# Kernel tuning notes

Measured on AMD Instinct MI355X. Metric: run time of the kernel, lower is better.

## Reference

```python
import jax, jax.numpy as jnp
import numpy as np

N_CLASS = 5      # episode way
SHOTS = 5        # support images per class
D = 64           # local descriptor dim (feature_dim)
H = W = 16       # feature map spatial size
N_QUERY = 75     # 15 queries per class


def setup_inputs() -> dict:
    key = jax.random.key(0)
    k1, k2 = jax.random.split(key)
    support = jax.random.normal(k1, (N_CLASS * SHOTS, D, H, W), dtype=jnp.float32)
    query = jax.random.normal(k2, (N_QUERY, D, H, W), dtype=jnp.float32)
    return {"support": support, "query": query, "task_index": 0, "k": 3, "k2": 64}


def reference(support, query, task_index, k, k2):
    C = N_CLASS
    n, d, h, w = support.shape
    hw = h * w
    ns = n // C  # shots per class

    # Per-class support descriptors: [C, ns*h*w, d], L2-normalized along d
    s = support.reshape(C, ns, d, hw)
    s = jnp.transpose(s, (0, 1, 3, 2)).reshape(C, ns * hw, d)
    s = s / jnp.linalg.norm(s, axis=-1, keepdims=True)

    # Query local descriptors: [B, d, Nq], L2-normalized along d
    B = query.shape[0]
    q = query.reshape(B, d, -1)
    q = q / jnp.linalg.norm(q, axis=1, keepdims=True)

    # Cosine similarity per class: [C, B, Nq, M]  (M = ns*h*w support descriptors)
    sim = jnp.einsum('cmd,bdq->cbqm', s, q)

    # torch.topk(sim, k, dim=1): top-k over support descriptors M per query location
    v = jax.lax.top_k(sim, k)[0]          # [C, B, Nq, k]
    v = jnp.swapaxes(v, 2, 3)             # [C, B, k, Nq]
    # torch.topk(., k2, dim=2): top-k2 over query locations
    v = jax.lax.top_k(v, k2)[0]           # [C, B, k, k2]

    # cat over classes, unsqueeze, then view(-1, 1, k, k2)
    return v.reshape(-1, 1, k, k2)        # [C*B, 1, k, k2]
```

## Files before the change

### kernel.cpp

```cpp
#include <hip/hip_runtime.h>
#include <stdint.h>


#define C_CLS 5
#define SHOTS 5
#define DIM 64
#define HW 256
#define NQ 75
#define K1 3
#define K2 64
#define M_TOT 1280
#define MPARTS 2
#define MPART 640
#define NIT 5
#define QBLK 128
#define NTILES 150

using bf16x8 = __attribute__((ext_vector_type(8))) short;
using f32x4  = __attribute__((ext_vector_type(4))) float;

typedef __attribute__((address_space(1))) const unsigned int GU32;
typedef __attribute__((address_space(3))) unsigned int LU32;

__device__ __forceinline__ void gload16(const void* g, void* l) {
    __builtin_amdgcn_global_load_lds((GU32*)g, (LU32*)l, 16, 0, 0);
}

#define SWZ(o) ((o) ^ ((((o) >> 7) & 7) << 4))

__device__ inline unsigned short f2bf(float x) {
    uint32_t u = __float_as_uint(x);
    u += 0x7FFF + ((u >> 16) & 1);
    return (unsigned short)(u >> 16);
}

__device__ __forceinline__ void ins3(float v, float& t0, float& t1, float& t2) {
    t2 = __builtin_amdgcn_fmed3f(v, t1, t2);
    t1 = __builtin_amdgcn_fmed3f(v, t0, t1);
    t0 = fmaxf(t0, v);
}

__global__ __launch_bounds__(256)
void prep(const float* __restrict__ support, const float* __restrict__ query,
          unsigned short* __restrict__ Sn, unsigned short* __restrict__ Qn) {
    const int tid  = threadIdx.x;
    const int wv   = tid >> 6, lane = tid & 63;
    const int dg   = lane >> 4, dl = lane & 15;
    const int bid  = blockIdx.x;
    const float* src;
    unsigned short* dst;
    if (bid < NQ * 4) {
        const int b    = bid >> 2;
        const int desc = (bid & 3) * 64 + wv * 16 + dl;
        src = query + (size_t)b * DIM * HW + desc;
        dst = Qn + ((size_t)b * HW + desc) * DIM + dg * 16;
    } else {
        const int sb   = bid - NQ * 4;
        const int cs   = sb >> 2;
        const int desc = (sb & 3) * 64 + wv * 16 + dl;
        const int c = cs / SHOTS, s = cs % SHOTS;
        src = support + (size_t)cs * DIM * HW + desc;
        dst = Sn + ((size_t)c * M_TOT + s * HW + desc) * DIM + dg * 16;
    }
    float v[16];
    float nrm = 0.f;
#pragma unroll
    for (int i = 0; i < 16; ++i) {
        const float x = src[(dg * 16 + i) * HW];
        v[i] = x; nrm = fmaf(x, x, nrm);
    }
    nrm += __shfl_xor(nrm, 16, 64);
    nrm += __shfl_xor(nrm, 32, 64);
    const float inv = rsqrtf(nrm);
    uint32_t p[8];
#pragma unroll
    for (int j = 0; j < 8; ++j)
        p[j] = (uint32_t)f2bf(v[2 * j] * inv) | ((uint32_t)f2bf(v[2 * j + 1] * inv) << 16);
    const uint4 w0 = {p[0], p[1], p[2], p[3]}, w1 = {p[4], p[5], p[6], p[7]};
    ((uint4*)dst)[0] = w0;
    ((uint4*)dst)[1] = w1;
}

__global__ __launch_bounds__(256, 6)
void dn4_mfma(const unsigned short* __restrict__ Sn,
              const unsigned short* __restrict__ Qn,
              unsigned short* __restrict__ partial) {
    __shared__ unsigned short sB[128 * DIM];

    const int tid  = threadIdx.x;
    const int lane = tid & 63, w = tid >> 6;
    const int c15  = lane & 15, kg = lane >> 4;
    const int bid  = blockIdx.x;
    const int c    = bid / 300;
    const int rem  = bid % 300;
    const int part = rem / NTILES;
    const int nt   = rem % NTILES;

    const int q0 = nt * QBLK + w * 32;
    bf16x8 aq[2][2];
#pragma unroll
    for (int g = 0; g < 2; ++g) {
        const unsigned short* qp = Qn + (size_t)(q0 + g * 16 + c15) * DIM + kg * 8;
        aq[g][0] = *(const bf16x8*)qp;
        aq[g][1] = *(const bf16x8*)(qp + 32);
    }

    float t0[2][4], t1[2][4], t2[2][4];
#pragma unroll
    for (int g = 0; g < 2; ++g)
#pragma unroll
        for (int r = 0; r < 4; ++r) { t0[g][r] = -2.f; t1[g][r] = -2.f; t2[g][r] = -2.f; }

    const int sw   = (c15 & 7) << 4;
    const int off0 = (kg * 16) ^ sw;
    const int off1 = (kg * 16 + 64) ^ sw;
    const int rowb = c15 * 128;

    const unsigned short* tb0 =
        Sn + ((size_t)c * M_TOT + part * MPART) * DIM;

    for (int it = 0; it < NIT; ++it) {
        __syncthreads();
        {
            const char* tb = (const char*)(tb0 + (size_t)it * 128 * DIM);
#pragma unroll
            for (int rep = 0; rep < 4; ++rep) {
                const int o = rep * 4096 + w * 1024 + lane * 16;
                gload16(tb + SWZ(o), (char*)sB + rep * 4096 + w * 1024);
            }
        }
        __syncthreads();

#pragma unroll
        for (int ns = 0; ns < 8; ++ns) {
            const char* rp = (const char*)sB + rowb + ns * 2048;
            const bf16x8 b0 = *(const bf16x8*)(rp + off0);
            const bf16x8 b1 = *(const bf16x8*)(rp + off1);
#pragma unroll
            for (int g = 0; g < 2; ++g) {
                f32x4 acc = {0.f, 0.f, 0.f, 0.f};
                acc = __builtin_amdgcn_mfma_f32_16x16x32_bf16(aq[g][0], b0, acc, 0, 0, 0);
                acc = __builtin_amdgcn_mfma_f32_16x16x32_bf16(aq[g][1], b1, acc, 0, 0, 0);
#pragma unroll
                for (int r = 0; r < 4; ++r)
                    ins3(acc[r], t0[g][r], t1[g][r], t2[g][r]);
            }
        }
    }

#pragma unroll
    for (int g = 0; g < 2; ++g)
#pragma unroll
        for (int r = 0; r < 4; ++r)
#pragma unroll
            for (int off = 1; off < 16; off <<= 1) {
                const float o0 = __shfl_xor(t0[g][r], off, 64);
                const float o1 = __shfl_xor(t1[g][r], off, 64);
                const float o2 = __shfl_xor(t2[g][r], off, 64);
                ins3(o0, t0[g][r], t1[g][r], t2[g][r]);
                ins3(o1, t0[g][r], t1[g][r], t2[g][r]);
                ins3(o2, t0[g][r], t1[g][r], t2[g][r]);
            }

    if (c15 == 0) {
        const int b = nt >> 1;
        unsigned short* pbase =
            partial + (((size_t)(c * NQ + b) * MPARTS + part) * K1) * HW;
#pragma unroll
        for (int g = 0; g < 2; ++g)
#pragma unroll
            for (int r = 0; r < 4; ++r) {
                const int qloc = (nt & 1) * QBLK + w * 32 + g * 16 + kg * 4 + r;
                pbase[qloc]          = f2bf(t0[g][r]);
                pbase[HW + qloc]     = f2bf(t1[g][r]);
                pbase[2 * HW + qloc] = f2bf(t2[g][r]);
            }
    }
}

__global__ __launch_bounds__(256)
void dn4_topq(const unsigned short* __restrict__ partial, float* __restrict__ out) {
    __shared__ float sbuf[HW];
    const int tid = threadIdx.x;
    const int bid = blockIdx.x;
    const int ki  = bid % K1;
    const int cb  = bid / K1;

    const unsigned short* p = partial + (size_t)cb * MPARTS * K1 * HW + tid;
    float t0 = -2.f, t1 = -2.f, t2 = -2.f;
#pragma unroll
    for (int h = 0; h < MPARTS; ++h)
#pragma unroll
        for (int r = 0; r < K1; ++r) {
            const float v = __uint_as_float((uint32_t)p[(h * K1 + r) * HW] << 16);
            ins3(v, t0, t1, t2);
        }
    float v = (ki == 0) ? t0 : (ki == 1) ? t1 : t2;

#pragma unroll
    for (int kk = 2; kk <= HW; kk <<= 1) {
#pragma unroll
        for (int j = kk >> 1; j > 0; j >>= 1) {
            const bool keep_max = (((tid & kk) == 0) == ((tid & j) == 0));
            float wv;
            if (j >= 64) {
                sbuf[tid] = v;
                __syncthreads();
                wv = sbuf[tid ^ j];
                __syncthreads();
            } else {
                wv = __shfl_xor(v, j, 64);
            }
            v = keep_max ? fmaxf(v, wv) : fminf(v, wv);
        }
    }
    if (tid < K2) out[(size_t)cb * K1 * K2 + (size_t)ki * K2 + tid] = v;
}

extern "C" void kernel_launch(void* const* d_in, const int* in_sizes, int n_in,
                              void* d_out, int out_size, void* d_ws, size_t ws_size,
                              hipStream_t stream) {
    const float* support = (const float*)d_in[0];
    const float* query   = (const float*)d_in[1];
    float* out = (float*)d_out;

    char* ws = (char*)d_ws;
    unsigned short* Sn      = (unsigned short*)ws;
    unsigned short* Qn      = (unsigned short*)(ws + 819200);
    unsigned short* partial = (unsigned short*)(ws + 819200 + 2457600);

    prep    <<<dim3(400),                      dim3(256), 0, stream>>>(support, query, Sn, Qn);
    dn4_mfma<<<dim3(C_CLS * MPARTS * NTILES),  dim3(256), 0, stream>>>(Sn, Qn, partial);
    dn4_topq<<<dim3(C_CLS * NQ * K1),          dim3(256), 0, stream>>>(partial, out);
}
```

Before: 46.40 us.

## Fuse similarity top-k and query top-k2 into one double-buffered kernel

Merges the MFMA similarity kernel and the query-location top-k2 kernel, so each block handles a full (class, query image) pair over all 1280 support descriptors. This removes the bf16 partial-results buffer, one kernel launch, and the M-split merge step. Support tiles are now double-buffered in LDS so the next tile's load overlaps the current tile's compute. The trade-off is far fewer blocks (375 instead of 1500 plus 1125), more registers per thread with QG=4, and three serial bitonic sorts per block.

```diff
diff --git a/kernel.cpp b/kernel.cpp
--- a/kernel.cpp
+++ b/kernel.cpp
@@ -10,11 +10,8 @@
 #define K1 3
 #define K2 64
 #define M_TOT 1280
-#define MPARTS 2
-#define MPART 640
-#define NIT 5
-#define QBLK 128
-#define NTILES 150
+#define NIT 10
+#define QG 4
 
 using bf16x8 = __attribute__((ext_vector_type(8))) short;
 using f32x4  = __attribute__((ext_vector_type(4))) float;
@@ -81,33 +78,30 @@
     ((uint4*)dst)[1] = w1;
 }
 
-__global__ __launch_bounds__(256, 6)
-void dn4_mfma(const unsigned short* __restrict__ Sn,
-              const unsigned short* __restrict__ Qn,
-              unsigned short* __restrict__ partial) {
-    __shared__ unsigned short sB[128 * DIM];
+__global__ __launch_bounds__(256)
+void dn4_fused(const unsigned short* __restrict__ Sn,
+               const unsigned short* __restrict__ Qn,
+               float* __restrict__ out) {
+    __shared__ unsigned short sB[2][128 * DIM];
 
     const int tid  = threadIdx.x;
     const int lane = tid & 63, w = tid >> 6;
     const int c15  = lane & 15, kg = lane >> 4;
     const int bid  = blockIdx.x;
-    const int c    = bid / 300;
-    const int rem  = bid % 300;
-    const int part = rem / NTILES;
-    const int nt   = rem % NTILES;
-
-    const int q0 = nt * QBLK + w * 32;
-    bf16x8 aq[2][2];
-#pragma unroll
-    for (int g = 0; g < 2; ++g) {
+    const int c    = bid / NQ, b = bid % NQ;
+
+    bf16x8 aq[QG][2];
+    const int q0 = b * HW + w * (QG * 16);
+#pragma unroll
+    for (int g = 0; g < QG; ++g) {
         const unsigned short* qp = Qn + (size_t)(q0 + g * 16 + c15) * DIM + kg * 8;
         aq[g][0] = *(const bf16x8*)qp;
         aq[g][1] = *(const bf16x8*)(qp + 32);
     }
 
-    float t0[2][4], t1[2][4], t2[2][4];
-#pragma unroll
-    for (int g = 0; g < 2; ++g)
+    float t0[QG][4], t1[QG][4], t2[QG][4];
+#pragma unroll
+    for (int g = 0; g < QG; ++g)
 #pragma unroll
         for (int r = 0; r < 4; ++r) { t0[g][r] = -2.f; t1[g][r] = -2.f; t2[g][r] = -2.f; }
 
@@ -116,28 +110,32 @@
     const int off1 = (kg * 16 + 64) ^ sw;
     const int rowb = c15 * 128;
 
-    const unsigned short* tb0 =
-        Sn + ((size_t)c * M_TOT + part * MPART) * DIM;
-
+    const char* tb0 = (const char*)(Sn + (size_t)c * M_TOT * DIM);
+
+#pragma unroll
+    for (int rep = 0; rep < 4; ++rep) {
+        const int o = rep * 4096 + tid * 16;
+        gload16(tb0 + SWZ(o), (char*)sB[0] + rep * 4096 + w * 1024);
+    }
+    __syncthreads();
+
+    int cur = 0;
     for (int it = 0; it < NIT; ++it) {
-        __syncthreads();
-        {
-            const char* tb = (const char*)(tb0 + (size_t)it * 128 * DIM);
+        if (it < NIT - 1) {
+            const char* tb = tb0 + (size_t)(it + 1) * 16384;
 #pragma unroll
             for (int rep = 0; rep < 4; ++rep) {
-                const int o = rep * 4096 + w * 1024 + lane * 16;
-                gload16(tb + SWZ(o), (char*)sB + rep * 4096 + w * 1024);
+                const int o = rep * 4096 + tid * 16;
+                gload16(tb + SWZ(o), (char*)sB[cur ^ 1] + rep * 4096 + w * 1024);
             }
         }
-        __syncthreads();
-
 #pragma unroll
         for (int ns = 0; ns < 8; ++ns) {
-            const char* rp = (const char*)sB + rowb + ns * 2048;
+            const char* rp = (const char*)sB[cur] + rowb + ns * 2048;
             const bf16x8 b0 = *(const bf16x8*)(rp + off0);
             const bf16x8 b1 = *(const bf16x8*)(rp + off1);
 #pragma unroll
-            for (int g = 0; g < 2; ++g) {
+            for (int g = 0; g < QG; ++g) {
                 f32x4 acc = {0.f, 0.f, 0.f, 0.f};
                 acc = __builtin_amdgcn_mfma_f32_16x16x32_bf16(aq[g][0], b0, acc, 0, 0, 0);
                 acc = __builtin_amdgcn_mfma_f32_16x16x32_bf16(aq[g][1], b1, acc, 0, 0, 0);
@@ -146,10 +144,12 @@
                     ins3(acc[r], t0[g][r], t1[g][r], t2[g][r]);
             }
         }
-    }
-
-#pragma unroll
-    for (int g = 0; g < 2; ++g)
+        __syncthreads();
+        cur ^= 1;
+    }
+
+#pragma unroll
+    for (int g = 0; g < QG; ++g)
 #pragma unroll
         for (int r = 0; r < 4; ++r)
 #pragma unroll
@@ -162,59 +162,43 @@
                 ins3(o2, t0[g][r], t1[g][r], t2[g][r]);
             }
 
+    float* sr = (float*)sB;
+    float* xb = sr + K1 * HW;
     if (c15 == 0) {
-        const int b = nt >> 1;
-        unsigned short* pbase =
-            partial + (((size_t)(c * NQ + b) * MPARTS + part) * K1) * HW;
-#pragma unroll
-        for (int g = 0; g < 2; ++g)
+#pragma unroll
+        for (int g = 0; g < QG; ++g)
 #pragma unroll
             for (int r = 0; r < 4; ++r) {
-                const int qloc = (nt & 1) * QBLK + w * 32 + g * 16 + kg * 4 + r;
-                pbase[qloc]          = f2bf(t0[g][r]);
-                pbase[HW + qloc]     = f2bf(t1[g][r]);
-                pbase[2 * HW + qloc] = f2bf(t2[g][r]);
-            }
-    }
-}
-
-__global__ __launch_bounds__(256)
-void dn4_topq(const unsigned short* __restrict__ partial, float* __restrict__ out) {
-    __shared__ float sbuf[HW];
-    const int tid = threadIdx.x;
-    const int bid = blockIdx.x;
-    const int ki  = bid % K1;
-    const int cb  = bid / K1;
-
-    const unsigned short* p = partial + (size_t)cb * MPARTS * K1 * HW + tid;
-    float t0 = -2.f, t1 = -2.f, t2 = -2.f;
-#pragma unroll
-    for (int h = 0; h < MPARTS; ++h)
-#pragma unroll
-        for (int r = 0; r < K1; ++r) {
-            const float v = __uint_as_float((uint32_t)p[(h * K1 + r) * HW] << 16);
-            ins3(v, t0, t1, t2);
+                const int qloc = w * (QG * 16) + g * 16 + kg * 4 + r;
+                sr[0 * HW + qloc] = t0[g][r];
+                sr[1 * HW + qloc] = t1[g][r];
+                sr[2 * HW + qloc] = t2[g][r];
+            }
+    }
+    __syncthreads();
+
+    const size_t obase = (size_t)bid * K1 * K2;
+    for (int rk = 0; rk < K1; ++rk) {
+        float v = sr[rk * HW + tid];
+#pragma unroll
+        for (int kk = 2; kk <= HW; kk <<= 1) {
+#pragma unroll
+            for (int j = kk >> 1; j > 0; j >>= 1) {
+                const bool keep_max = (((tid & kk) == 0) == ((tid & j) == 0));
+                float pw;
+                if (j >= 64) {
+                    xb[tid] = v;
+                    __syncthreads();
+                    pw = xb[tid ^ j];
+                    __syncthreads();
+                } else {
+                    pw = __shfl_xor(v, j, 64);
+                }
+                v = keep_max ? fmaxf(v, pw) : fminf(v, pw);
+            }
         }
-    float v = (ki == 0) ? t0 : (ki == 1) ? t1 : t2;
-
-#pragma unroll
-    for (int kk = 2; kk <= HW; kk <<= 1) {
-#pragma unroll
-        for (int j = kk >> 1; j > 0; j >>= 1) {
-            const bool keep_max = (((tid & kk) == 0) == ((tid & j) == 0));
-            float wv;
-            if (j >= 64) {
-                sbuf[tid] = v;
-                __syncthreads();
-                wv = sbuf[tid ^ j];
-                __syncthreads();
-            } else {
-                wv = __shfl_xor(v, j, 64);
-            }
-            v = keep_max ? fmaxf(v, wv) : fminf(v, wv);
-        }
-    }
-    if (tid < K2) out[(size_t)cb * K1 * K2 + (size_t)ki * K2 + tid] = v;
+        if (tid < K2) out[obase + (size_t)rk * K2 + tid] = v;
+    }
 }
 
 extern "C" void kernel_launch(void* const* d_in, const int* in_sizes, int n_in,
@@ -225,11 +209,9 @@
     float* out = (float*)d_out;
 
     char* ws = (char*)d_ws;
-    unsigned short* Sn      = (unsigned short*)ws;
-    unsigned short* Qn      = (unsigned short*)(ws + 819200);
-    unsigned short* partial = (unsigned short*)(ws + 819200 + 2457600);
-
-    prep    <<<dim3(400),                      dim3(256), 0, stream>>>(support, query, Sn, Qn);
-    dn4_mfma<<<dim3(C_CLS * MPARTS * NTILES),  dim3(256), 0, stream>>>(Sn, Qn, partial);
-    dn4_topq<<<dim3(C_CLS * NQ * K1),          dim3(256), 0, stream>>>(partial, out);
-}
+    unsigned short* Sn = (unsigned short*)ws;
+    unsigned short* Qn = (unsigned short*)(ws + 819200);
+
+    prep     <<<dim3(400),          dim3(256), 0, stream>>>(support, query, Sn, Qn);
+    dn4_fused<<<dim3(C_CLS * NQ),   dim3(256), 0, stream>>>(Sn, Qn, out);
+}
```

Result: slower. 54.15 us (+16.7%).

## Double-buffer support tiles and split support rows four ways with 512-thread blocks

Applied to the files above, without the earlier changes.

The similarity kernel now uses 512-thread blocks that each cover a whole query image (256 locations) against a quarter of a class's support descriptors. It prefetches the next 64-row support tile into a second LDS buffer while the current tile feeds the MFMAs, so each iteration needs one barrier instead of two. The top-k reduction now merges four partial top-3 lists instead of two. This is meant to hide global-to-LDS latency and raise support-tile reuse across more query rows, at the cost of more partial output and a larger merge step.

```diff
diff --git a/kernel.cpp b/kernel.cpp
--- a/kernel.cpp
+++ b/kernel.cpp
@@ -10,11 +10,11 @@
 #define K1 3
 #define K2 64
 #define M_TOT 1280
-#define MPARTS 2
-#define MPART 640
-#define NIT 5
-#define QBLK 128
-#define NTILES 150
+#define MQ 4
+#define MQROWS (M_TOT / MQ)
+#define TROWS 64
+#define NIT (MQROWS / TROWS)
+#define QG 2
 
 using bf16x8 = __attribute__((ext_vector_type(8))) short;
 using f32x4  = __attribute__((ext_vector_type(4))) float;
@@ -81,33 +81,32 @@
     ((uint4*)dst)[1] = w1;
 }
 
-__global__ __launch_bounds__(256, 6)
+__global__ __launch_bounds__(512)
 void dn4_mfma(const unsigned short* __restrict__ Sn,
               const unsigned short* __restrict__ Qn,
               unsigned short* __restrict__ partial) {
-    __shared__ unsigned short sB[128 * DIM];
+    __shared__ unsigned short sB[2][TROWS * DIM];
 
     const int tid  = threadIdx.x;
     const int lane = tid & 63, w = tid >> 6;
     const int c15  = lane & 15, kg = lane >> 4;
     const int bid  = blockIdx.x;
-    const int c    = bid / 300;
-    const int rem  = bid % 300;
-    const int part = rem / NTILES;
-    const int nt   = rem % NTILES;
-
-    const int q0 = nt * QBLK + w * 32;
-    bf16x8 aq[2][2];
-#pragma unroll
-    for (int g = 0; g < 2; ++g) {
+    const int b    = bid % NQ;
+    const int cq   = bid / NQ;
+    const int c    = cq >> 2, qt = cq & 3;
+
+    bf16x8 aq[QG][2];
+    const int q0 = b * HW + w * (QG * 16);
+#pragma unroll
+    for (int g = 0; g < QG; ++g) {
         const unsigned short* qp = Qn + (size_t)(q0 + g * 16 + c15) * DIM + kg * 8;
         aq[g][0] = *(const bf16x8*)qp;
         aq[g][1] = *(const bf16x8*)(qp + 32);
     }
 
-    float t0[2][4], t1[2][4], t2[2][4];
-#pragma unroll
-    for (int g = 0; g < 2; ++g)
+    float t0[QG][4], t1[QG][4], t2[QG][4];
+#pragma unroll
+    for (int g = 0; g < QG; ++g)
 #pragma unroll
         for (int r = 0; r < 4; ++r) { t0[g][r] = -2.f; t1[g][r] = -2.f; t2[g][r] = -2.f; }
 
@@ -116,28 +115,24 @@
     const int off1 = (kg * 16 + 64) ^ sw;
     const int rowb = c15 * 128;
 
-    const unsigned short* tb0 =
-        Sn + ((size_t)c * M_TOT + part * MPART) * DIM;
-
+    const char* tb0 = (const char*)(Sn + ((size_t)c * M_TOT + qt * MQROWS) * DIM);
+
+    gload16(tb0 + SWZ(tid * 16), (char*)sB[0] + w * 1024);
+    __syncthreads();
+
+    int cur = 0;
     for (int it = 0; it < NIT; ++it) {
-        __syncthreads();
-        {
-            const char* tb = (const char*)(tb0 + (size_t)it * 128 * DIM);
-#pragma unroll
-            for (int rep = 0; rep < 4; ++rep) {
-                const int o = rep * 4096 + w * 1024 + lane * 16;
-                gload16(tb + SWZ(o), (char*)sB + rep * 4096 + w * 1024);
-            }
-        }
-        __syncthreads();
-
-#pragma unroll
-        for (int ns = 0; ns < 8; ++ns) {
-            const char* rp = (const char*)sB + rowb + ns * 2048;
+        if (it < NIT - 1) {
+            const char* tb = tb0 + (size_t)(it + 1) * (TROWS * DIM * 2);
+            gload16(tb + SWZ(tid * 16), (char*)sB[cur ^ 1] + w * 1024);
+        }
+#pragma unroll
+        for (int ns = 0; ns < 4; ++ns) {
+            const char* rp = (const char*)sB[cur] + rowb + ns * 2048;
             const bf16x8 b0 = *(const bf16x8*)(rp + off0);
             const bf16x8 b1 = *(const bf16x8*)(rp + off1);
 #pragma unroll
-            for (int g = 0; g < 2; ++g) {
+            for (int g = 0; g < QG; ++g) {
                 f32x4 acc = {0.f, 0.f, 0.f, 0.f};
                 acc = __builtin_amdgcn_mfma_f32_16x16x32_bf16(aq[g][0], b0, acc, 0, 0, 0);
                 acc = __builtin_amdgcn_mfma_f32_16x16x32_bf16(aq[g][1], b1, acc, 0, 0, 0);
@@ -146,10 +141,12 @@
                     ins3(acc[r], t0[g][r], t1[g][r], t2[g][r]);
             }
         }
-    }
-
-#pragma unroll
-    for (int g = 0; g < 2; ++g)
+        __syncthreads();
+        cur ^= 1;
+    }
+
+#pragma unroll
+    for (int g = 0; g < QG; ++g)
 #pragma unroll
         for (int r = 0; r < 4; ++r)
 #pragma unroll
@@ -163,14 +160,13 @@
             }
 
     if (c15 == 0) {
-        const int b = nt >> 1;
         unsigned short* pbase =
-            partial + (((size_t)(c * NQ + b) * MPARTS + part) * K1) * HW;
-#pragma unroll
-        for (int g = 0; g < 2; ++g)
+            partial + (((size_t)(c * NQ + b) * MQ + qt) * K1) * HW;
+#pragma unroll
+        for (int g = 0; g < QG; ++g)
 #pragma unroll
             for (int r = 0; r < 4; ++r) {
-                const int qloc = (nt & 1) * QBLK + w * 32 + g * 16 + kg * 4 + r;
+                const int qloc = w * (QG * 16) + g * 16 + kg * 4 + r;
                 pbase[qloc]          = f2bf(t0[g][r]);
                 pbase[HW + qloc]     = f2bf(t1[g][r]);
                 pbase[2 * HW + qloc] = f2bf(t2[g][r]);
@@ -186,10 +182,10 @@
     const int ki  = bid % K1;
     const int cb  = bid / K1;
 
-    const unsigned short* p = partial + (size_t)cb * MPARTS * K1 * HW + tid;
+    const unsigned short* p = partial + (size_t)cb * MQ * K1 * HW + tid;
     float t0 = -2.f, t1 = -2.f, t2 = -2.f;
 #pragma unroll
-    for (int h = 0; h < MPARTS; ++h)
+    for (int h = 0; h < MQ; ++h)
 #pragma unroll
         for (int r = 0; r < K1; ++r) {
             const float v = __uint_as_float((uint32_t)p[(h * K1 + r) * HW] << 16);
@@ -229,7 +225,7 @@
     unsigned short* Qn      = (unsigned short*)(ws + 819200);
     unsigned short* partial = (unsigned short*)(ws + 819200 + 2457600);
 
-    prep    <<<dim3(400),                      dim3(256), 0, stream>>>(support, query, Sn, Qn);
-    dn4_mfma<<<dim3(C_CLS * MPARTS * NTILES),  dim3(256), 0, stream>>>(Sn, Qn, partial);
-    dn4_topq<<<dim3(C_CLS * NQ * K1),          dim3(256), 0, stream>>>(partial, out);
-}
+    prep    <<<dim3(400),               dim3(256), 0, stream>>>(support, query, Sn, Qn);
+    dn4_mfma<<<dim3(C_CLS * MQ * NQ),   dim3(512), 0, stream>>>(Sn, Qn, partial);
+    dn4_topq<<<dim3(C_CLS * NQ * K1),   dim3(256), 0, stream>>>(partial, out);
+}
```

Result: slower. 51.06 us (+10.0%).
